# Performance work log

Measured on AMD Instinct MI355X. Metric: run time of the kernel, lower is better.

## Reference

```python
import jax, jax.numpy as jnp
import numpy as np

B, C, N, H = 16, 256, 2048, 128


def setup_inputs() -> dict:
    key = jax.random.key(0)
    ks = jax.random.split(key, 9)
    s_in = 1.0 / np.sqrt(C)
    s_h = 1.0 / np.sqrt(H)
    return {
        "x": jax.random.normal(ks[0], (B, C, N), dtype=jnp.float32),
        "Wq": jax.random.uniform(ks[1], (H, C), jnp.float32, -s_in, s_in),
        "bq": jax.random.uniform(ks[2], (H,), jnp.float32, -s_in, s_in),
        "Wk": jax.random.uniform(ks[3], (H, C), jnp.float32, -s_in, s_in),
        "bk": jax.random.uniform(ks[4], (H,), jnp.float32, -s_in, s_in),
        "Wv": jax.random.uniform(ks[5], (H, C), jnp.float32, -s_in, s_in),
        "bv": jax.random.uniform(ks[6], (H,), jnp.float32, -s_in, s_in),
        "Wf": jax.random.uniform(ks[7], (C, H), jnp.float32, -s_h, s_h),
        "bf": jax.random.uniform(ks[8], (C,), jnp.float32, -s_h, s_h),
    }


def reference(x, Wq, bq, Wk, bk, Wv, bv, Wf, bf):
    # 1x1 conv == channel-wise linear: [B,C,N] -> [B,H,N]
    Q = jnp.einsum("bcn,hc->bhn", x, Wq) + bq[:, None]
    K = jnp.einsum("bcn,hc->bhn", x, Wk) + bk[:, None]
    V = jnp.einsum("bcn,hc->bhn", x, Wv) + bv[:, None]
    # attn[b, i, j] = softmax_j( Q[b,:,i] . K[b,:,j] )   (no sqrt(d) scaling, as in source)
    scores = jnp.einsum("bhi,bhj->bij", Q, K)          # [B, N, N]
    attn = jax.nn.softmax(scores, axis=-1)
    # out[b, h, i] = sum_j V[b,h,j] * attn[b,i,j]
    out = jnp.einsum("bhj,bij->bhi", V, attn)           # [B, H, N]
    out = jnp.einsum("bhn,ch->bcn", out, Wf) + bf[:, None]
    return out + x
```

## Files before the change

### kernel.cpp

```cpp
#include <hip/hip_runtime.h>
#include <hip/hip_bf16.h>

#define BATCH 16
#define CDIM 256
#define NDIM 2048
#define HDIM 128
#define KVB 64
#define NT (NDIM / KVB)

typedef __bf16 bf16;
typedef float f32x4 __attribute__((ext_vector_type(4)));
typedef float f32x16 __attribute__((ext_vector_type(16)));
typedef bf16 bf16x8 __attribute__((ext_vector_type(8)));
typedef unsigned int u32x4 __attribute__((ext_vector_type(4)));
typedef unsigned int u32x2 __attribute__((ext_vector_type(2)));

#define LOG2E 1.4426950408889634f

__device__ __forceinline__ int swz512(int row, int colbyte) {
  return row * 512 + (colbyte ^ ((row & 15) << 4));
}
__device__ __forceinline__ int swz256(int row, int colbyte) {
  return row * 256 + (colbyte ^ ((row & 7) << 4));
}

__device__ __forceinline__ f32x4 mfma16(bf16x8 a, bf16x8 b, f32x4 c) {
  return __builtin_amdgcn_mfma_f32_16x16x32_bf16(a, b, c, 0, 0, 0);
}
__device__ __forceinline__ f32x16 mfma32(bf16x8 a, bf16x8 b, f32x16 c) {
  return __builtin_amdgcn_mfma_f32_32x32x16_bf16(a, b, c, 0, 0, 0);
}

__device__ __forceinline__ unsigned cvtpk(float lo, float hi) {
  unsigned r;
  asm("v_cvt_pk_bf16_f32 %0, %1, %2" : "=v"(r) : "v"(lo), "v"(hi));
  return r;
}
__device__ __forceinline__ void pswap(unsigned &a, unsigned &b) {
  asm volatile("v_permlane32_swap_b32 %0, %1" : "+v"(a), "+v"(b));
}

__device__ __forceinline__ void gload16(const bf16* g, char* l) {
  __builtin_amdgcn_global_load_lds(
      (const __attribute__((address_space(1))) void*)g,
      (__attribute__((address_space(3))) void*)l, 16, 0, 0);
}

__device__ __forceinline__ bf16x8 cvt8(float4 a, float4 b) {
  bf16x8 o;
  o[0] = (bf16)a.x; o[1] = (bf16)a.y; o[2] = (bf16)a.z; o[3] = (bf16)a.w;
  o[4] = (bf16)b.x; o[5] = (bf16)b.y; o[6] = (bf16)b.z; o[7] = (bf16)b.w;
  return o;
}

__global__ __launch_bounds__(256) void k1_qkv(
    const float* __restrict__ x,
    const float* __restrict__ Wq, const float* __restrict__ bq,
    const float* __restrict__ Wk, const float* __restrict__ bk,
    const float* __restrict__ Wv, const float* __restrict__ bv,
    bf16* __restrict__ Qo, bf16* __restrict__ Ko, bf16* __restrict__ Vo) {
  __shared__ char lds[65536];
  char* xT = lds;
  char* Wt = lds + 32768;

  const int t = threadIdx.x;
  const int l = t & 63;
  const int w = t >> 6;
  const int q = (l >> 4) & 3;
  const int b = blockIdx.x >> 5;
  const int n0 = (blockIdx.x & 31) * 64;

#pragma unroll
  for (int p = 0; p < 16; ++p) {
    int c = w * 64 + p * 4 + q;
    float4 v = *reinterpret_cast<const float4*>(
        x + (size_t)(b * CDIM + c) * NDIM + n0 + (l & 15) * 4);
    float t0 = __shfl_xor(v.x, 16), t1 = __shfl_xor(v.y, 16);
    float t2 = __shfl_xor(v.z, 16), t3 = __shfl_xor(v.w, 16);
    float4 wv;
    if ((q & 1) == 0) wv = make_float4(v.x, t0, v.z, t2);
    else              wv = make_float4(t1, v.y, t3, v.w);
    float s0 = __shfl_xor(wv.x, 32), s1 = __shfl_xor(wv.y, 32);
    float s2 = __shfl_xor(wv.z, 32), s3 = __shfl_xor(wv.w, 32);
    float4 z;
    if ((q & 2) == 0) z = make_float4(wv.x, wv.y, s0, s1);
    else              z = make_float4(s2, s3, wv.z, wv.w);
    u32x2 pk = {cvtpk(z.x, z.y), cvtpk(z.z, z.w)};
    int n = (l & 15) * 4 + q;
    int slot = w * 8 + (p >> 1);
    *reinterpret_cast<u32x2*>(
        xT + n * 512 + ((slot ^ (n & 15)) * 16 + (p & 1) * 8)) = pk;
  }

  const float* Wp[3] = {Wq, Wk, Wv};
  const float* bp[3] = {bq, bk, bv};

#pragma unroll 1
  for (int p = 0; p < 3; ++p) {
    f32x4 acc[8];
#pragma unroll
    for (int i = 0; i < 8; ++i) acc[i] = f32x4{0.f, 0.f, 0.f, 0.f};

#pragma unroll 1
    for (int kh = 0; kh < 2; ++kh) {
      __syncthreads();
#pragma unroll
      for (int pass = 0; pass < 8; ++pass) {
        int h = pass * 16 + (t >> 4);
        int cq = t & 15;
        const float* src = Wp[p] + (size_t)h * CDIM + kh * 128 + cq * 8;
        float4 v0 = *reinterpret_cast<const float4*>(src);
        float4 v1 = *reinterpret_cast<const float4*>(src + 4);
        *reinterpret_cast<bf16x8*>(Wt + swz256(h, cq * 16)) = cvt8(v0, v1);
      }
      __syncthreads();

      if (p < 2) {
#pragma unroll
        for (int ks = 0; ks < 4; ++ks) {
          int cb2 = ks * 64 + (l >> 4) * 16;
          bf16x8 a = *reinterpret_cast<const bf16x8*>(
              xT + swz512(w * 16 + (l & 15), kh * 256 + cb2));
#pragma unroll
          for (int nf = 0; nf < 8; ++nf) {
            bf16x8 bb = *reinterpret_cast<const bf16x8*>(
                Wt + swz256(nf * 16 + (l & 15), cb2));
            acc[nf] = mfma16(a, bb, acc[nf]);
          }
        }
      } else {
#pragma unroll
        for (int ks = 0; ks < 4; ++ks) {
          int cb2 = ks * 64 + (l >> 4) * 16;
          bf16x8 a0 = *reinterpret_cast<const bf16x8*>(
              Wt + swz256(w * 32 + (l & 15), cb2));
          bf16x8 a1 = *reinterpret_cast<const bf16x8*>(
              Wt + swz256(w * 32 + 16 + (l & 15), cb2));
#pragma unroll
          for (int nf = 0; nf < 4; ++nf) {
            bf16x8 bb = *reinterpret_cast<const bf16x8*>(
                xT + swz512(nf * 16 + (l & 15), kh * 256 + cb2));
            acc[nf] = mfma16(a0, bb, acc[nf]);
            acc[4 + nf] = mfma16(a1, bb, acc[4 + nf]);
          }
        }
      }
    }

    if (p < 2) {
      bf16* dst = (p == 0) ? Qo : Ko;
      const float scale = (p == 0) ? LOG2E : 1.0f;
#pragma unroll
      for (int nf = 0; nf < 8; ++nf) {
        float bias = bp[p][nf * 16 + (l & 15)];
#pragma unroll
        for (int r = 0; r < 4; ++r) {
          int n = n0 + w * 16 + (l >> 4) * 4 + r;
          int h = nf * 16 + (l & 15);
          dst[(size_t)(b * NDIM + n) * HDIM + h] = (bf16)((acc[nf][r] + bias) * scale);
        }
      }
    } else {
#pragma unroll
      for (int mf = 0; mf < 2; ++mf)
#pragma unroll
        for (int nf = 0; nf < 4; ++nf)
#pragma unroll
          for (int r = 0; r < 4; ++r) {
            int h = w * 32 + mf * 16 + (l >> 4) * 4 + r;
            int n = n0 + nf * 16 + (l & 15);
            Vo[(size_t)(b * HDIM + h) * NDIM + n] =
                (bf16)(acc[mf * 4 + nf][r] + bp[2][h]);
          }
    }
  }
}

__global__ __launch_bounds__(256, 2) void k2_attn(
    const bf16* __restrict__ Q, const bf16* __restrict__ K,
    const bf16* __restrict__ V, bf16* __restrict__ O) {
  extern __shared__ char lds[];

  const int t = threadIdx.x;
  const int l = t & 63;
  const int w = t >> 6;
  const int wm = w & 1;
  const int wk = w >> 1;
  const int hi = l >> 5;
  const int c31 = l & 31;

  const int pid = blockIdx.x;
  const int b = (pid & 7) * 2 + ((pid >> 3) >> 5);
  const int q0 = ((pid >> 3) & 31) * 64;

  bf16x8 qf[8];
  {
    const bf16* qb = Q + ((size_t)b * NDIM + q0 + wm * 32 + c31) * HDIM + hi * 8;
#pragma unroll
    for (int cs = 0; cs < 8; ++cs)
      qf[cs] = *reinterpret_cast<const bf16x8*>(qb + cs * 16);
  }

  unsigned offK[4], offV[4];
  {
    const int krow = w * 16 + (l >> 4);
    const int kslot = l & 15;
#pragma unroll
    for (int i = 0; i < 4; ++i) {
      int r = krow + i * 4;
      offK[i] = (unsigned)((b * NDIM + r) * HDIM + (kslot ^ (r & 15)) * 8);
    }
    const int vrow = w * 32 + (l >> 3);
    const int vslot = l & 7;
#pragma unroll
    for (int i = 0; i < 4; ++i) {
      int r = vrow + i * 8;
      offV[i] = (unsigned)((b * HDIM + r) * NDIM + (vslot ^ (r & 7)) * 8);
    }
  }
  const int kbase = w * 4096;
  const int vbase = 16384 + w * 4096;

  f32x16 oacc[4];
#pragma unroll
  for (int dg = 0; dg < 4; ++dg)
#pragma unroll
    for (int r = 0; r < 16; ++r) oacc[dg][r] = 0.f;
  float l_run = 0.f;

#pragma unroll
  for (int i = 0; i < 4; ++i) gload16(K + offK[i], lds + kbase + i * 1024);
#pragma unroll
  for (int i = 0; i < 4; ++i) gload16(V + offV[i], lds + vbase + i * 1024);

  const int krow = wk * 32 + c31;
  const int rxk = krow & 15;
  const int rxv = c31 & 7;

#pragma unroll 1
  for (int kt = 0; kt < NT; ++kt) {
    char* buf = lds + (kt & 1) * 32768;
    if (kt + 1 < NT) {
      char* nbuf = lds + ((kt + 1) & 1) * 32768;
#pragma unroll
      for (int i = 0; i < 4; ++i) {
        offK[i] += (unsigned)(KVB * HDIM);
        gload16(K + offK[i], nbuf + kbase + i * 1024);
      }
#pragma unroll
      for (int i = 0; i < 4; ++i) {
        offV[i] += (unsigned)KVB;
        gload16(V + offV[i], nbuf + vbase + i * 1024);
      }
      asm volatile("s_waitcnt vmcnt(8)" ::: "memory");
    } else {
      asm volatile("s_waitcnt vmcnt(0)" ::: "memory");
    }
    __builtin_amdgcn_s_barrier();

    const char* Kt = buf;
    const char* Vt = buf + 16384;

    f32x16 s;
#pragma unroll
    for (int r = 0; r < 16; ++r) s[r] = 0.f;
    __builtin_amdgcn_s_setprio(1);
    {
      const char* kr = Kt + krow * 256;
#pragma unroll
      for (int cs = 0; cs < 8; ++cs) {
        bf16x8 kf = *reinterpret_cast<const bf16x8*>(
            kr + (((cs * 2 + hi) ^ rxk) * 16));
        s = mfma32(kf, qf[cs], s);
      }
    }
    __builtin_amdgcn_s_setprio(0);

    bf16x8 vf[8];
#pragma unroll
    for (int dg = 0; dg < 4; ++dg) {
      const char* vr = Vt + (dg * 32 + c31) * 128;
      vf[2 * dg + 0] = *reinterpret_cast<const bf16x8*>(
          vr + (((wk * 4 + 0 + hi) ^ rxv) * 16));
      vf[2 * dg + 1] = *reinterpret_cast<const bf16x8*>(
          vr + (((wk * 4 + 2 + hi) ^ rxv) * 16));
    }

#pragma unroll
    for (int r = 0; r < 16; ++r) s[r] = __builtin_amdgcn_exp2f(s[r]);
    {
      float a0 = s[0] + s[1], a1 = s[2] + s[3], a2 = s[4] + s[5], a3 = s[6] + s[7];
      float a4 = s[8] + s[9], a5 = s[10] + s[11], a6 = s[12] + s[13], a7 = s[14] + s[15];
      float b0 = a0 + a1, b1 = a2 + a3, b2 = a4 + a5, b3 = a6 + a7;
      l_run += (b0 + b1) + (b2 + b3);
    }

    unsigned w0 = cvtpk(s[0], s[1]);
    unsigned w1 = cvtpk(s[2], s[3]);
    unsigned w2 = cvtpk(s[4], s[5]);
    unsigned w3 = cvtpk(s[6], s[7]);
    unsigned w4 = cvtpk(s[8], s[9]);
    unsigned w5 = cvtpk(s[10], s[11]);
    unsigned w6 = cvtpk(s[12], s[13]);
    unsigned w7 = cvtpk(s[14], s[15]);
    pswap(w0, w2); pswap(w1, w3); pswap(w4, w6); pswap(w5, w7);
    u32x4 pw0 = {w0, w1, w2, w3};
    u32x4 pw1 = {w4, w5, w6, w7};
    bf16x8 pa0 = __builtin_bit_cast(bf16x8, pw0);
    bf16x8 pa1 = __builtin_bit_cast(bf16x8, pw1);

    __builtin_amdgcn_s_setprio(1);
#pragma unroll
    for (int dg = 0; dg < 4; ++dg) {
      oacc[dg] = mfma32(pa0, vf[2 * dg + 0], oacc[dg]);
      oacc[dg] = mfma32(pa1, vf[2 * dg + 1], oacc[dg]);
    }
    __builtin_amdgcn_s_setprio(0);
    __builtin_amdgcn_s_barrier();
  }

  l_run += __shfl_xor(l_run, 32);
  float* O1 = (float*)lds;
  float* L1 = (float*)(lds + 32768);
  if (wk == 1) {
#pragma unroll
    for (int dg = 0; dg < 4; ++dg)
#pragma unroll
      for (int r = 0; r < 16; ++r)
        O1[wm * 4096 + (dg * 16 + r) * 64 + l] = oacc[dg][r];
    if (l < 32) L1[wm * 32 + c31] = l_run;
  }
  __syncthreads();
  if (wk == 0) {
    float linv = 1.0f / (l_run + L1[wm * 32 + c31]);
    int ibits = __builtin_bit_cast(int, linv);
#pragma unroll
    for (int dg = 0; dg < 4; ++dg) {
      int h = dg * 32 + c31;
#pragma unroll
      for (int r = 0; r < 16; ++r) {
        int crow = (r & 3) + 8 * (r >> 2) + 4 * hi;
        float fr = __builtin_bit_cast(
            float, __builtin_amdgcn_ds_bpermute(crow * 4, ibits));
        float val = (oacc[dg][r] + O1[wm * 4096 + (dg * 16 + r) * 64 + l]) * fr;
        int n = q0 + wm * 32 + crow;
        O[((size_t)b * NDIM + n) * HDIM + h] = (bf16)val;
      }
    }
  }
}

__global__ __launch_bounds__(256) void k3_proj(
    const bf16* __restrict__ O, const float* __restrict__ Wf,
    const float* __restrict__ bfv, const float* __restrict__ x,
    float* __restrict__ out) {
  __shared__ char lds[49152];
  char* Wt = lds;
  char* Ot = lds + 32768;

  const int t = threadIdx.x;
  const int l = t & 63;
  const int w = t >> 6;
  const int b = blockIdx.x >> 5;
  const int n0 = (blockIdx.x & 31) * 64;

#pragma unroll
  for (int pass = 0; pass < 4; ++pass) {
    int n = pass * 16 + (t >> 4);
    int hq = t & 15;
    uint4 d = *reinterpret_cast<const uint4*>(
        O + (size_t)(b * NDIM + n0 + n) * HDIM + hq * 8);
    *reinterpret_cast<uint4*>(Ot + swz256(n, hq * 16)) = d;
  }

#pragma unroll 1
  for (int ch = 0; ch < 2; ++ch) {
    __syncthreads();
#pragma unroll
    for (int pass = 0; pass < 8; ++pass) {
      int cl = pass * 16 + (t >> 4);
      int hq = t & 15;
      const float* src = Wf + (size_t)(ch * 128 + cl) * HDIM + hq * 8;
      float4 v0 = *reinterpret_cast<const float4*>(src);
      float4 v1 = *reinterpret_cast<const float4*>(src + 4);
      *reinterpret_cast<bf16x8*>(Wt + swz256(cl, hq * 16)) = cvt8(v0, v1);
    }
    __syncthreads();

    f32x4 acc[2][4];
#pragma unroll
    for (int i = 0; i < 2; ++i)
#pragma unroll
      for (int j = 0; j < 4; ++j) acc[i][j] = f32x4{0.f, 0.f, 0.f, 0.f};

#pragma unroll
    for (int ks = 0; ks < 4; ++ks) {
      int cb = ks * 64 + (l >> 4) * 16;
      bf16x8 a0 = *reinterpret_cast<const bf16x8*>(
          Wt + swz256(w * 32 + (l & 15), cb));
      bf16x8 a1 = *reinterpret_cast<const bf16x8*>(
          Wt + swz256(w * 32 + 16 + (l & 15), cb));
#pragma unroll
      for (int nf = 0; nf < 4; ++nf) {
        bf16x8 bb = *reinterpret_cast<const bf16x8*>(
            Ot + swz256(nf * 16 + (l & 15), cb));
        acc[0][nf] = mfma16(a0, bb, acc[0][nf]);
        acc[1][nf] = mfma16(a1, bb, acc[1][nf]);
      }
    }

#pragma unroll
    for (int mf = 0; mf < 2; ++mf)
#pragma unroll
      for (int nf = 0; nf < 4; ++nf)
#pragma unroll
        for (int r = 0; r < 4; ++r) {
          int c = ch * 128 + w * 32 + mf * 16 + (l >> 4) * 4 + r;
          int n = n0 + nf * 16 + (l & 15);
          size_t idx = (size_t)(b * CDIM + c) * NDIM + n;
          out[idx] = acc[mf][nf][r] + bfv[c] + x[idx];
        }
  }
}

extern "C" void kernel_launch(void* const* d_in, const int* in_sizes, int n_in,
                              void* d_out, int out_size, void* d_ws,
                              size_t ws_size, hipStream_t stream) {
  (void)in_sizes; (void)n_in; (void)out_size;
  const float* x = (const float*)d_in[0];
  const float* Wq = (const float*)d_in[1];
  const float* bq = (const float*)d_in[2];
  const float* Wk = (const float*)d_in[3];
  const float* bk = (const float*)d_in[4];
  const float* Wv = (const float*)d_in[5];
  const float* bv = (const float*)d_in[6];
  const float* Wf = (const float*)d_in[7];
  const float* bfv = (const float*)d_in[8];
  float* out = (float*)d_out;

  if (ws_size < (24u << 20)) return;
  char* ws = (char*)d_ws;
  bf16* Qb = (bf16*)(ws);
  bf16* Kb = (bf16*)(ws + (8u << 20));
  bf16* Vb = (bf16*)(ws + (16u << 20));

  const unsigned k2_lds = 65536;
  hipFuncSetAttribute(reinterpret_cast<const void*>(k2_attn),
                      hipFuncAttributeMaxDynamicSharedMemorySize, (int)k2_lds);

  k1_qkv<<<512, 256, 0, stream>>>(x, Wq, bq, Wk, bk, Wv, bv, Qb, Kb, Vb);
  k2_attn<<<512, 256, k2_lds, stream>>>(Qb, Kb, Vb, Qb);
  k3_proj<<<512, 256, 0, stream>>>(Qb, Wf, bfv, x, out);
}
```

Measured before the change: 98.71 us.

## Prepack QKV weights to bf16 and double-buffer async weight loads into LDS

A new small kernel converts Wq/Wk/Wv to bf16 once, writing them into the tail of the output buffer as scratch. k1 then streams the packed weights in quarter-K chunks with global_load_lds into two alternating LDS buffers, prefetching the next chunk while running MFMAs on the current one. This removes the per-block fp32 weight loads and conversions and the synchronous staging stalls. The cost is an extra kernel launch, and the output buffer is used as temporary storage that k3 overwrites later.

```diff
diff --git a/kernel.cpp b/kernel.cpp
--- a/kernel.cpp
+++ b/kernel.cpp
@@ -53,15 +53,27 @@
   return o;
 }
 
+__global__ __launch_bounds__(256) void k0_pack(
+    const float* __restrict__ Wq, const float* __restrict__ Wk,
+    const float* __restrict__ Wv, bf16* __restrict__ Wpk) {
+  int g = blockIdx.x * 256 + threadIdx.x;
+  int p = g >> 12;
+  int e = (g & 4095) * 8;
+  const float* W = (p == 0) ? Wq : (p == 1 ? Wk : Wv);
+  float4 v0 = *reinterpret_cast<const float4*>(W + e);
+  float4 v1 = *reinterpret_cast<const float4*>(W + e + 4);
+  *reinterpret_cast<bf16x8*>(Wpk + p * 32768 + e) = cvt8(v0, v1);
+}
+
 __global__ __launch_bounds__(256) void k1_qkv(
-    const float* __restrict__ x,
-    const float* __restrict__ Wq, const float* __restrict__ bq,
-    const float* __restrict__ Wk, const float* __restrict__ bk,
-    const float* __restrict__ Wv, const float* __restrict__ bv,
+    const float* __restrict__ x, const bf16* __restrict__ Wpk,
+    const float* __restrict__ bq, const float* __restrict__ bk,
+    const float* __restrict__ bv,
     bf16* __restrict__ Qo, bf16* __restrict__ Ko, bf16* __restrict__ Vo) {
-  __shared__ char lds[65536];
-  char* xT = lds;
-  char* Wt = lds + 32768;
+  __shared__ char lds_[65536];
+  char* xT = lds_;
+  char* wb0 = lds_ + 32768;
+  char* wb1 = lds_ + 49152;
 
   const int t = threadIdx.x;
   const int l = t & 63;
@@ -69,6 +81,13 @@
   const int q = (l >> 4) & 3;
   const int b = blockIdx.x >> 5;
   const int n0 = (blockIdx.x & 31) * 64;
+
+  const int lane_off = (l >> 3) * 256 + (((l & 7) ^ (l >> 3)) * 8);
+
+#pragma unroll
+  for (int i = 0; i < 4; ++i)
+    gload16(Wpk + 0 * 32768 + 0 * 64 + i * 8192 + w * 2048 + lane_off,
+            wb0 + i * 4096 + w * 1024);
 
 #pragma unroll
   for (int p = 0; p < 16; ++p) {
@@ -91,88 +110,95 @@
     *reinterpret_cast<u32x2*>(
         xT + n * 512 + ((slot ^ (n & 15)) * 16 + (p & 1) * 8)) = pk;
   }
-
-  const float* Wp[3] = {Wq, Wk, Wv};
-  const float* bp[3] = {bq, bk, bv};
+  asm volatile("s_waitcnt lgkmcnt(0)" ::: "memory");
+
+  f32x4 acc[8];
+  const float* bias_p[3] = {bq, bk, bv};
 
 #pragma unroll 1
-  for (int p = 0; p < 3; ++p) {
-    f32x4 acc[8];
-#pragma unroll
-    for (int i = 0; i < 8; ++i) acc[i] = f32x4{0.f, 0.f, 0.f, 0.f};
-
-#pragma unroll 1
-    for (int kh = 0; kh < 2; ++kh) {
-      __syncthreads();
-#pragma unroll
-      for (int pass = 0; pass < 8; ++pass) {
-        int h = pass * 16 + (t >> 4);
-        int cq = t & 15;
-        const float* src = Wp[p] + (size_t)h * CDIM + kh * 128 + cq * 8;
-        float4 v0 = *reinterpret_cast<const float4*>(src);
-        float4 v1 = *reinterpret_cast<const float4*>(src + 4);
-        *reinterpret_cast<bf16x8*>(Wt + swz256(h, cq * 16)) = cvt8(v0, v1);
-      }
-      __syncthreads();
-
+  for (int r = 0; r < 12; ++r) {
+    const int p = r >> 2, kq = r & 3;
+    char* wb = (r & 1) ? wb1 : wb0;
+    if ((r & 3) == 0) {
+#pragma unroll
+      for (int i = 0; i < 8; ++i) acc[i] = f32x4{0.f, 0.f, 0.f, 0.f};
+    }
+    if (r + 1 < 12) {
+      const int p1 = (r + 1) >> 2, kq1 = (r + 1) & 3;
+      char* nwb = (r & 1) ? wb0 : wb1;
+      const bf16* src = Wpk + p1 * 32768 + kq1 * 64 + w * 2048 + lane_off;
+#pragma unroll
+      for (int i = 0; i < 4; ++i)
+        gload16(src + i * 8192, nwb + i * 4096 + w * 1024);
+      asm volatile("s_waitcnt vmcnt(4)" ::: "memory");
+    } else {
+      asm volatile("s_waitcnt vmcnt(0)" ::: "memory");
+    }
+    __builtin_amdgcn_s_barrier();
+
+    if (p < 2) {
+#pragma unroll
+      for (int ks = 0; ks < 2; ++ks) {
+        int cb = kq * 128 + ks * 64 + (l >> 4) * 16;
+        bf16x8 a = *reinterpret_cast<const bf16x8*>(
+            xT + swz512(w * 16 + (l & 15), cb));
+        int slot = ((ks * 4 + (l >> 4)) ^ (l & 7)) * 16;
+#pragma unroll
+        for (int nf = 0; nf < 8; ++nf) {
+          bf16x8 bb = *reinterpret_cast<const bf16x8*>(
+              wb + (nf * 16 + (l & 15)) * 128 + slot);
+          acc[nf] = mfma16(a, bb, acc[nf]);
+        }
+      }
+    } else {
+#pragma unroll
+      for (int ks = 0; ks < 2; ++ks) {
+        int slot = ((ks * 4 + (l >> 4)) ^ (l & 7)) * 16;
+        bf16x8 a0 = *reinterpret_cast<const bf16x8*>(
+            wb + (w * 32 + (l & 15)) * 128 + slot);
+        bf16x8 a1 = *reinterpret_cast<const bf16x8*>(
+            wb + (w * 32 + 16 + (l & 15)) * 128 + slot);
+        int cb = kq * 128 + ks * 64 + (l >> 4) * 16;
+#pragma unroll
+        for (int nf4 = 0; nf4 < 4; ++nf4) {
+          bf16x8 bx = *reinterpret_cast<const bf16x8*>(
+              xT + swz512(nf4 * 16 + (l & 15), cb));
+          acc[nf4] = mfma16(a0, bx, acc[nf4]);
+          acc[4 + nf4] = mfma16(a1, bx, acc[4 + nf4]);
+        }
+      }
+    }
+
+    if ((r & 3) == 3) {
       if (p < 2) {
-#pragma unroll
-        for (int ks = 0; ks < 4; ++ks) {
-          int cb2 = ks * 64 + (l >> 4) * 16;
-          bf16x8 a = *reinterpret_cast<const bf16x8*>(
-              xT + swz512(w * 16 + (l & 15), kh * 256 + cb2));
-#pragma unroll
-          for (int nf = 0; nf < 8; ++nf) {
-            bf16x8 bb = *reinterpret_cast<const bf16x8*>(
-                Wt + swz256(nf * 16 + (l & 15), cb2));
-            acc[nf] = mfma16(a, bb, acc[nf]);
+        bf16* dst = (p == 0) ? Qo : Ko;
+        const float scale = (p == 0) ? LOG2E : 1.0f;
+#pragma unroll
+        for (int nf = 0; nf < 8; ++nf) {
+          float bias = bias_p[p][nf * 16 + (l & 15)];
+#pragma unroll
+          for (int rr = 0; rr < 4; ++rr) {
+            int n = n0 + w * 16 + (l >> 4) * 4 + rr;
+            int h = nf * 16 + (l & 15);
+            dst[(size_t)(b * NDIM + n) * HDIM + h] =
+                (bf16)((acc[nf][rr] + bias) * scale);
           }
         }
       } else {
 #pragma unroll
-        for (int ks = 0; ks < 4; ++ks) {
-          int cb2 = ks * 64 + (l >> 4) * 16;
-          bf16x8 a0 = *reinterpret_cast<const bf16x8*>(
-              Wt + swz256(w * 32 + (l & 15), cb2));
-          bf16x8 a1 = *reinterpret_cast<const bf16x8*>(
-              Wt + swz256(w * 32 + 16 + (l & 15), cb2));
-#pragma unroll
-          for (int nf = 0; nf < 4; ++nf) {
-            bf16x8 bb = *reinterpret_cast<const bf16x8*>(
-                xT + swz512(nf * 16 + (l & 15), kh * 256 + cb2));
-            acc[nf] = mfma16(a0, bb, acc[nf]);
-            acc[4 + nf] = mfma16(a1, bb, acc[4 + nf]);
-          }
-        }
-      }
-    }
-
-    if (p < 2) {
-      bf16* dst = (p == 0) ? Qo : Ko;
-      const float scale = (p == 0) ? LOG2E : 1.0f;
-#pragma unroll
-      for (int nf = 0; nf < 8; ++nf) {
-        float bias = bp[p][nf * 16 + (l & 15)];
-#pragma unroll
-        for (int r = 0; r < 4; ++r) {
-          int n = n0 + w * 16 + (l >> 4) * 4 + r;
-          int h = nf * 16 + (l & 15);
-          dst[(size_t)(b * NDIM + n) * HDIM + h] = (bf16)((acc[nf][r] + bias) * scale);
-        }
-      }
-    } else {
-#pragma unroll
-      for (int mf = 0; mf < 2; ++mf)
-#pragma unroll
-        for (int nf = 0; nf < 4; ++nf)
-#pragma unroll
-          for (int r = 0; r < 4; ++r) {
-            int h = w * 32 + mf * 16 + (l >> 4) * 4 + r;
-            int n = n0 + nf * 16 + (l & 15);
-            Vo[(size_t)(b * HDIM + h) * NDIM + n] =
-                (bf16)(acc[mf * 4 + nf][r] + bp[2][h]);
-          }
-    }
+        for (int mf = 0; mf < 2; ++mf)
+#pragma unroll
+          for (int nf4 = 0; nf4 < 4; ++nf4)
+#pragma unroll
+            for (int rr = 0; rr < 4; ++rr) {
+              int h = w * 32 + mf * 16 + (l >> 4) * 4 + rr;
+              int n = n0 + nf4 * 16 + (l & 15);
+              Vo[(size_t)(b * HDIM + h) * NDIM + n] =
+                  (bf16)(acc[mf * 4 + nf4][rr] + bv[h]);
+            }
+      }
+    }
+    __builtin_amdgcn_s_barrier();
   }
 }
 
@@ -426,7 +452,7 @@
 extern "C" void kernel_launch(void* const* d_in, const int* in_sizes, int n_in,
                               void* d_out, int out_size, void* d_ws,
                               size_t ws_size, hipStream_t stream) {
-  (void)in_sizes; (void)n_in; (void)out_size;
+  (void)in_sizes; (void)n_in;
   const float* x = (const float*)d_in[0];
   const float* Wq = (const float*)d_in[1];
   const float* bq = (const float*)d_in[2];
@@ -444,11 +470,15 @@
   bf16* Kb = (bf16*)(ws + (8u << 20));
   bf16* Vb = (bf16*)(ws + (16u << 20));
 
+  const size_t out_bytes = (size_t)out_size * 4;
+  bf16* Wpk = (bf16*)((char*)d_out + out_bytes - 196608);
+
   const unsigned k2_lds = 65536;
   hipFuncSetAttribute(reinterpret_cast<const void*>(k2_attn),
                       hipFuncAttributeMaxDynamicSharedMemorySize, (int)k2_lds);
 
-  k1_qkv<<<512, 256, 0, stream>>>(x, Wq, bq, Wk, bk, Wv, bv, Qb, Kb, Vb);
+  k0_pack<<<48, 256, 0, stream>>>(Wq, Wk, Wv, Wpk);
+  k1_qkv<<<512, 256, 0, stream>>>(x, Wpk, bq, bk, bv, Qb, Kb, Vb);
   k2_attn<<<512, 256, k2_lds, stream>>>(Qb, Kb, Vb, Qb);
   k3_proj<<<512, 256, 0, stream>>>(Qb, Wf, bfv, x, out);
 }
```

New measurement: 91.69 us. -7.1%, faster.
